# Optimization experiments

Hardware: AMD Instinct MI355X
Metric: run time of the kernel (lower is better)

Reference implementation:

```python
import jax, jax.numpy as jnp
import numpy as np
from jax import lax

H = 128  # LSTM hidden size (hardcoded in module)

def setup_inputs() -> dict:
    key = jax.random.key(0)
    ks = jax.random.split(key, 10)
    B, S, D = 256, 512, 80
    T = 3
    s_in = 1.0 / np.sqrt(D)
    s_h = 1.0 / np.sqrt(H)
    return {
        "x": jax.random.normal(ks[0], (B, S, D), dtype=jnp.float32),
        "W_in": jax.random.uniform(ks[1], (256, D), jnp.float32, -s_in, s_in),
        "b_in": jax.random.uniform(ks[2], (256,), jnp.float32, -s_in, s_in),
        "W_ih": jax.random.uniform(ks[3], (4 * H, 256), jnp.float32, -s_h, s_h),
        "b_ih": jax.random.uniform(ks[4], (4 * H,), jnp.float32, -s_h, s_h),
        "W_hh": jax.random.uniform(ks[5], (4 * H, H), jnp.float32, -s_h, s_h),
        "b_hh": jax.random.uniform(ks[6], (4 * H,), jnp.float32, -s_h, s_h),
        "w_time": jax.random.uniform(ks[7], (T,), jnp.float32, -1.0 / np.sqrt(T), 1.0 / np.sqrt(T)),
        "W_br": jax.random.uniform(ks[8], (4, H), jnp.float32, -s_h, s_h),
        "b_br": jax.random.uniform(ks[9], (4,), jnp.float32, -s_h, s_h),
        "batch_size": B,
        "time_steps": T,
    }


def reference(x, W_in, b_in, W_ih, b_ih, W_hh, b_hh, w_time, W_br, b_br, batch_size, time_steps):
    # input projection (dropout is identity in eval mode)
    xl = jnp.einsum('bsd,ed->bse', x, W_in) + b_in  # [B,S,256]
    B, S, _ = xl.shape
    T = time_steps

    def step(carry, inp):
        h, c, h_st, c_st = carry
        xt, i = inp  # xt: [B,256], i: step index
        gates = xt @ W_ih.T + b_ih + h @ W_hh.T + b_hh  # [B,4H]
        ig, fg, gg, og = jnp.split(gates, 4, axis=-1)
        c_new = jax.nn.sigmoid(fg) * c + jax.nn.sigmoid(ig) * jnp.tanh(gg)
        h_new = jax.nn.sigmoid(og) * jnp.tanh(c_new)
        slot = i % T
        oh = jax.nn.one_hot(slot, T, dtype=h_new.dtype)  # [T]
        h_st = h_st * (1.0 - oh) + h_new[:, :, None] * oh  # [B,H,T]
        c_st = c_st * (1.0 - oh) + c_new[:, :, None] * oh
        pool = (slot == T - 1)
        ph = jnp.einsum('bht,t->bh', h_st, w_time)
        pc = jnp.einsum('bht,t->bh', c_st, w_time)
        h_out = jnp.where(pool, ph, h_new)
        c_out = jnp.where(pool, pc, c_new)
        h_st = jnp.where(pool, jnp.zeros_like(h_st), h_st)
        c_st = jnp.where(pool, jnp.zeros_like(c_st), c_st)
        return (h_out, c_out, h_st, c_st), h_out

    init = (jnp.zeros((B, H), xl.dtype), jnp.zeros((B, H), xl.dtype),
            jnp.zeros((B, H, T), xl.dtype), jnp.zeros((B, H, T), xl.dtype))
    _, outs = lax.scan(step, init, (jnp.swapaxes(xl, 0, 1), jnp.arange(S)))
    out = jnp.swapaxes(outs, 0, 1)  # [B,S,H]
    logits = jnp.einsum('bsh,oh->bso', out, W_br) + b_br  # [B,S,4]
    return jax.nn.log_softmax(logits, axis=2)
```

## Files before the change

### kernel.cpp

```cpp
#include <hip/hip_runtime.h>
#include <hip/hip_fp16.h>

#define BB 256
#define SS 512
#define DD 80
#define HH 128
#define GG 512

typedef _Float16 h2_t __attribute__((ext_vector_type(2)));

union U32H2 { unsigned int u; h2_t h; unsigned short us[2]; };

static __device__ __forceinline__ h2_t u2h(unsigned int u) { U32H2 x; x.u = u; return x.h; }

static __device__ __forceinline__ unsigned int pk2(float a, float b) {
  unsigned int lo = (unsigned int)__half_as_ushort(__float2half(a));
  unsigned int hi = (unsigned int)__half_as_ushort(__float2half(b));
  return (hi << 16) | lo;
}

static __device__ __forceinline__ float fdot2(unsigned int a, unsigned int b, float c) {
#if __has_builtin(__builtin_amdgcn_fdot2)
  return __builtin_amdgcn_fdot2(u2h(a), u2h(b), c, false);
#else
  U32H2 ua, ub; ua.u = a; ub.u = b;
  return c + (float)ua.h[0] * (float)ub.h[0] + (float)ua.h[1] * (float)ub.h[1];
#endif
}

static __device__ __forceinline__ float fsig(float x) {
  return __fdividef(1.f, 1.f + __expf(-x));
}

__global__ __launch_bounds__(128) void prep_kernel(
    const float* __restrict__ W_in, const float* __restrict__ b_in,
    const float* __restrict__ W_ih, const float* __restrict__ b_ih,
    const float* __restrict__ W_hh, const float* __restrict__ b_hh,
    unsigned short* __restrict__ wc16, unsigned short* __restrict__ whh16,
    float* __restrict__ biasc)
{
  const int g = blockIdx.x;
  const int t = threadIdx.x;
  const float* wih = W_ih + g * 256;
  if (t < DD) {
    float s = 0.f;
    for (int e = 0; e < 256; ++e) s += wih[e] * W_in[e * DD + t];
    wc16[g * DD + t] = __half_as_ushort(__float2half(s));
  }
  whh16[g * HH + t] = __half_as_ushort(__float2half(W_hh[g * HH + t]));
  if (t == 0) {
    float s = 0.f;
    for (int e = 0; e < 256; ++e) s += wih[e] * b_in[e];
    biasc[g] = s + b_ih[g] + b_hh[g];
  }
}

__global__ __launch_bounds__(256) void gemm_kernel(
    const float* __restrict__ x,
    const unsigned short* __restrict__ wc16,
    uint4* __restrict__ gx)
{
  __shared__ unsigned int Al[40][64];
  __shared__ unsigned int Bl[40][256];
  const int t  = threadIdx.x;
  const int mt = blockIdx.x;
  const int g0 = blockIdx.y * 256;

  {
    const int mm = t & 63, kq = t >> 6;
    const float* xr = x + ((size_t)mt * 64 + mm) * DD + kq * 20;
    #pragma unroll
    for (int p = 0; p < 10; ++p)
      Al[kq * 10 + p][mm] = pk2(xr[2 * p], xr[2 * p + 1]);
  }
  {
    const unsigned int* wr = (const unsigned int*)wc16 + (size_t)(g0 + t) * 40;
    #pragma unroll
    for (int k = 0; k < 40; ++k) Bl[k][t] = wr[k];
  }
  __syncthreads();

  const int mb = (t >> 5) * 8;
  const int gb = (t & 31) * 4;
  float acc[8][8];
  #pragma unroll
  for (int i = 0; i < 8; ++i)
    #pragma unroll
    for (int j = 0; j < 8; ++j) acc[i][j] = 0.f;

  #pragma unroll 5
  for (int kk = 0; kk < 40; ++kk) {
    uint4 a0 = *(const uint4*)&Al[kk][mb];
    uint4 a1 = *(const uint4*)&Al[kk][mb + 4];
    uint4 b0 = *(const uint4*)&Bl[kk][gb];
    uint4 b1 = *(const uint4*)&Bl[kk][gb + 128];
    unsigned int aa[8] = {a0.x, a0.y, a0.z, a0.w, a1.x, a1.y, a1.z, a1.w};
    unsigned int bb[8] = {b0.x, b0.y, b0.z, b0.w, b1.x, b1.y, b1.z, b1.w};
    #pragma unroll
    for (int i = 0; i < 8; ++i)
      #pragma unroll
      for (int j = 0; j < 8; ++j)
        acc[i][j] = fdot2(aa[i], bb[j], acc[i][j]);
  }

  const size_t rb = (size_t)mt * 8 + (t >> 5);
  #pragma unroll
  for (int jj = 0; jj < 2; ++jj) {
    #pragma unroll
    for (int j = 0; j < 4; ++j) {
      const int jc = jj * 4 + j;
      uint4 o;
      o.x = pk2(acc[0][jc], acc[1][jc]);
      o.y = pk2(acc[2][jc], acc[3][jc]);
      o.z = pk2(acc[4][jc], acc[5][jc]);
      o.w = pk2(acc[6][jc], acc[7][jc]);
      gx[rb * 512 + (size_t)(g0 + jj * 128 + gb + j)] = o;
    }
  }
}

__global__ __launch_bounds__(256, 1) void scan_kernel(
    const uint4* __restrict__ gx,
    const uint4* __restrict__ whh,
    const float* __restrict__ biasc,
    const float* __restrict__ wtime,
    __half* __restrict__ hout)
{
  __shared__ unsigned int hbuf[2][64];
  const int b    = blockIdx.x;
  const int t    = threadIdx.x;
  const int lane = t & 63;
  const int hi   = t >> 1;
  const int odd  = t & 1;
  const int g1   = odd * 128 + hi;
  const int g2   = g1 + 256;

  unsigned int w1[64], w2[64];
  {
    const uint4* wr1 = whh + (size_t)g1 * 16;
    const uint4* wr2 = whh + (size_t)g2 * 16;
    #pragma unroll
    for (int i = 0; i < 16; ++i) {
      uint4 v = wr1[i];
      w1[4*i] = v.x; w1[4*i+1] = v.y; w1[4*i+2] = v.z; w1[4*i+3] = v.w;
      uint4 u = wr2[i];
      w2[4*i] = u.x; w2[4*i+1] = u.y; w2[4*i+2] = u.z; w2[4*i+3] = u.w;
    }
  }
  const float bias1 = biasc[g1];
  const float bias2 = biasc[g2];
  const float wt0 = wtime[0], wt1 = wtime[1], wt2 = wtime[2];
  if (t < 64) { hbuf[0][t] = 0u; hbuf[1][t] = 0u; }
  float c = 0.f, hst0 = 0.f, hst1 = 0.f, cst0 = 0.f, cst1 = 0.f;
  int slot = 0, s = 0;
  const uint4* gxp1 = gx + (size_t)b * 64 * 512 + g1;
  const uint4* gxp2 = gx + (size_t)b * 64 * 512 + g2;
  __syncthreads();

  uint4 gv1 = gxp1[0];
  uint4 gv2 = gxp2[0];
  for (int sb = 0; sb < 64; ++sb) {
    uint4 gn1, gn2;
    if (sb < 63) {
      gn1 = gxp1[(size_t)(sb + 1) * 512];
      gn2 = gxp2[(size_t)(sb + 1) * 512];
    }
    unsigned int ga1[4] = {gv1.x, gv1.y, gv1.z, gv1.w};
    unsigned int ga2[4] = {gv2.x, gv2.y, gv2.z, gv2.w};
    #pragma unroll
    for (int i = 0; i < 8; ++i) {
      const int par = s & 1;
      const unsigned int hreg = hbuf[par][lane];
      U32H2 u1; u1.u = ga1[i >> 1];
      U32H2 u2; u2.u = ga2[i >> 1];
      const float gxi1 = (float)u1.h[i & 1];
      const float gxi2 = (float)u2.h[i & 1];
      float d1a = bias1 + gxi1, d1b = 0.f;
      float d2a = bias2 + gxi2, d2b = 0.f;
      #pragma unroll
      for (int p = 0; p < 64; p += 2) {
        unsigned int h0 = (unsigned int)__builtin_amdgcn_readlane((int)hreg, p);
        unsigned int h1 = (unsigned int)__builtin_amdgcn_readlane((int)hreg, p + 1);
        d1a = fdot2(w1[p],     h0, d1a);
        d2a = fdot2(w2[p],     h0, d2a);
        d1b = fdot2(w1[p + 1], h1, d1b);
        d2b = fdot2(w2[p + 1], h1, d2b);
      }
      const float d1 = d1a + d1b;
      const float d2 = d2a + d2b;
      const float a1 = fsig(d1);
      const float yin = odd ? d2 : (d2 + d2);
      const float sv  = fsig(yin);
      const float a2  = odd ? sv : (2.f * sv - 1.f);
      const float p1 = __shfl_xor(a1, 1);
      const float p2 = __shfl_xor(a2, 1);
      const float iv = odd ? p1 : a1;
      const float gg = odd ? p2 : a2;
      const float fv = odd ? a1 : p1;
      const float ov = odd ? a2 : p2;
      c = fv * c + iv * gg;
      const float tc = 2.f * fsig(c + c) - 1.f;
      const float hn = ov * tc;
      float hcur;
      if (slot == 2) {
        hcur = hst0 * wt0 + hst1 * wt1 + hn * wt2;
        c    = cst0 * wt0 + cst1 * wt1 + c  * wt2;
        slot = 0;
      } else {
        hcur = hn;
        if (slot == 0) { hst0 = hn; cst0 = c; }
        else           { hst1 = hn; cst1 = c; }
        ++slot;
      }
      if (!odd) {
        const __half hh = __float2half(hcur);
        ((__half*)hbuf[par ^ 1])[hi] = hh;
        hout[((size_t)b * SS + s) * HH + hi] = hh;
      }
      ++s;
      __syncthreads();
    }
    gv1 = gn1;
    gv2 = gn2;
  }
}

__global__ __launch_bounds__(256) void out_kernel(
    const uint4* __restrict__ hout,
    const float* __restrict__ Wbr, const float* __restrict__ bbr,
    float4* __restrict__ out)
{
  __shared__ unsigned int wb[4][64];
  __shared__ float bbs[4];
  const int t = threadIdx.x;
  {
    const int o = t >> 6, p = t & 63;
    wb[o][p] = pk2(Wbr[o * HH + 2 * p], Wbr[o * HH + 2 * p + 1]);
  }
  if (t < 4) bbs[t] = bbr[t];
  __syncthreads();

  const size_t row = (size_t)blockIdx.x * 256 + t;
  const uint4* hr = hout + row * 16;
  float a0 = bbs[0], a1 = bbs[1], a2 = bbs[2], a3 = bbs[3];
  #pragma unroll
  for (int q = 0; q < 16; ++q) {
    uint4 hv = hr[q];
    unsigned int hd[4] = {hv.x, hv.y, hv.z, hv.w};
    #pragma unroll
    for (int d = 0; d < 4; ++d) {
      const int p = q * 4 + d;
      a0 = fdot2(hd[d], wb[0][p], a0);
      a1 = fdot2(hd[d], wb[1][p], a1);
      a2 = fdot2(hd[d], wb[2][p], a2);
      a3 = fdot2(hd[d], wb[3][p], a3);
    }
  }
  const float m = fmaxf(fmaxf(a0, a1), fmaxf(a2, a3));
  const float e0 = __expf(a0 - m), e1 = __expf(a1 - m), e2 = __expf(a2 - m), e3 = __expf(a3 - m);
  const float lse = m + __logf(e0 + e1 + e2 + e3);
  out[row] = make_float4(a0 - lse, a1 - lse, a2 - lse, a3 - lse);
}

extern "C" void kernel_launch(void* const* d_in, const int* in_sizes, int n_in,
                              void* d_out, int out_size, void* d_ws, size_t ws_size,
                              hipStream_t stream) {
  const float* x     = (const float*)d_in[0];
  const float* W_in  = (const float*)d_in[1];
  const float* b_in  = (const float*)d_in[2];
  const float* W_ih  = (const float*)d_in[3];
  const float* b_ih  = (const float*)d_in[4];
  const float* W_hh  = (const float*)d_in[5];
  const float* b_hh  = (const float*)d_in[6];
  const float* wtime = (const float*)d_in[7];
  const float* W_br  = (const float*)d_in[8];
  const float* b_br  = (const float*)d_in[9];
  (void)in_sizes; (void)n_in; (void)out_size; (void)ws_size;

  char* ws = (char*)d_ws;
  unsigned short* wc16  = (unsigned short*)(ws + 0);
  unsigned short* whh16 = (unsigned short*)(ws + 81920);
  float*          biasc = (float*)(ws + 212992);
  __half*         hout  = (__half*)(ws + 215040);
  uint4*          gx    = (uint4*)(ws + 33769472);

  prep_kernel<<<512, 128, 0, stream>>>(W_in, b_in, W_ih, b_ih, W_hh, b_hh,
                                       wc16, whh16, biasc);
  gemm_kernel<<<dim3(2048, 2), 256, 0, stream>>>(x, wc16, gx);
  scan_kernel<<<256, 256, 0, stream>>>(gx, (const uint4*)whh16, biasc, wtime, hout);
  out_kernel<<<512, 256, 0, stream>>>((const uint4*)hout, W_br, b_br, (float4*)d_out);
}
```

Baseline: 609.3 us.

## Rewrite input-gate GEMM with MFMA 16x16x32 f16 instructions

Replaces the fdot2-based register-tiled input projection GEMM with one that uses MFMA 16x16x32 f16 instructions. Shared memory is re-laid row-major with K padded from 80 to 96 using zeros, loads become vectorized float4/uint4, and each block now covers 128 gate columns across a grid twice as wide. Output packing uses a lane shuffle to keep the same interleaved gx layout. The scan kernel's occupancy hint moves from launch_bounds min-blocks to amdgpu_waves_per_eu(1,1). The GEMM is a small part of total time next to the sequential scan, so the overall effect is limited.

```diff
diff --git a/kernel.cpp b/kernel.cpp
--- a/kernel.cpp
+++ b/kernel.cpp
@@ -8,6 +8,8 @@
 #define GG 512
 
 typedef _Float16 h2_t __attribute__((ext_vector_type(2)));
+typedef _Float16 half8 __attribute__((ext_vector_type(8)));
+typedef float f32x4 __attribute__((ext_vector_type(4)));
 
 union U32H2 { unsigned int u; h2_t h; unsigned short us[2]; };
 
@@ -57,69 +59,78 @@
 
 __global__ __launch_bounds__(256) void gemm_kernel(
     const float* __restrict__ x,
-    const unsigned short* __restrict__ wc16,
+    const unsigned int* __restrict__ wc,
     uint4* __restrict__ gx)
 {
-  __shared__ unsigned int Al[40][64];
-  __shared__ unsigned int Bl[40][256];
+  __shared__ unsigned int Al[64 * 52];
+  __shared__ unsigned int Bl[128 * 52];
   const int t  = threadIdx.x;
   const int mt = blockIdx.x;
-  const int g0 = blockIdx.y * 256;
+  const int g0 = blockIdx.y * 128;
 
   {
-    const int mm = t & 63, kq = t >> 6;
-    const float* xr = x + ((size_t)mt * 64 + mm) * DD + kq * 20;
-    #pragma unroll
-    for (int p = 0; p < 10; ++p)
-      Al[kq * 10 + p][mm] = pk2(xr[2 * p], xr[2 * p + 1]);
+    const float4* xr = (const float4*)(x + (size_t)mt * 64 * DD);
+    #pragma unroll
+    for (int i = 0; i < 5; ++i) {
+      int f = t + i * 256;
+      int row = f / 20, c4 = f % 20;
+      float4 v = xr[row * 20 + c4];
+      Al[row * 52 + c4 * 2]     = pk2(v.x, v.y);
+      Al[row * 52 + c4 * 2 + 1] = pk2(v.z, v.w);
+    }
+    #pragma unroll
+    for (int i = 0; i < 3; ++i) {
+      int f = t + i * 256;
+      int row = f / 12, c = f % 12;
+      Al[row * 52 + 40 + c] = 0u;
+    }
   }
   {
-    const unsigned int* wr = (const unsigned int*)wc16 + (size_t)(g0 + t) * 40;
-    #pragma unroll
-    for (int k = 0; k < 40; ++k) Bl[k][t] = wr[k];
+    #pragma unroll
+    for (int i = 0; i < 5; ++i) {
+      int f = t + i * 256;
+      int row = f / 10, c4 = f % 10;
+      uint4 v = *(const uint4*)(wc + (size_t)(g0 + row) * 40 + c4 * 4);
+      *(uint4*)&Bl[row * 52 + c4 * 4] = v;
+    }
+    #pragma unroll
+    for (int i = 0; i < 3; ++i) {
+      int f = t + i * 256;
+      int row = f / 12, c = f % 12;
+      Bl[row * 52 + 40 + c] = 0u;
+    }
   }
   __syncthreads();
 
-  const int mb = (t >> 5) * 8;
-  const int gb = (t & 31) * 4;
-  float acc[8][8];
+  const int w = t >> 6, lane = t & 63;
+  const int m = lane & 15, q = lane >> 4;
+
+  half8 af[3];
   #pragma unroll
-  for (int i = 0; i < 8; ++i)
-    #pragma unroll
-    for (int j = 0; j < 8; ++j) acc[i][j] = 0.f;
-
-  #pragma unroll 5
-  for (int kk = 0; kk < 40; ++kk) {
-    uint4 a0 = *(const uint4*)&Al[kk][mb];
-    uint4 a1 = *(const uint4*)&Al[kk][mb + 4];
-    uint4 b0 = *(const uint4*)&Bl[kk][gb];
-    uint4 b1 = *(const uint4*)&Bl[kk][gb + 128];
-    unsigned int aa[8] = {a0.x, a0.y, a0.z, a0.w, a1.x, a1.y, a1.z, a1.w};
-    unsigned int bb[8] = {b0.x, b0.y, b0.z, b0.w, b1.x, b1.y, b1.z, b1.w};
-    #pragma unroll
-    for (int i = 0; i < 8; ++i)
-      #pragma unroll
-      for (int j = 0; j < 8; ++j)
-        acc[i][j] = fdot2(aa[i], bb[j], acc[i][j]);
-  }
-
-  const size_t rb = (size_t)mt * 8 + (t >> 5);
+  for (int kk = 0; kk < 3; ++kk)
+    af[kk] = *(const half8*)((const char*)Al + (size_t)(w * 16 + m) * 208 + kk * 64 + q * 16);
+
   #pragma unroll
-  for (int jj = 0; jj < 2; ++jj) {
-    #pragma unroll
-    for (int j = 0; j < 4; ++j) {
-      const int jc = jj * 4 + j;
-      uint4 o;
-      o.x = pk2(acc[0][jc], acc[1][jc]);
-      o.y = pk2(acc[2][jc], acc[3][jc]);
-      o.z = pk2(acc[4][jc], acc[5][jc]);
-      o.w = pk2(acc[6][jc], acc[7][jc]);
-      gx[rb * 512 + (size_t)(g0 + jj * 128 + gb + j)] = o;
-    }
-  }
-}
-
-__global__ __launch_bounds__(256, 1) void scan_kernel(
+  for (int j = 0; j < 8; ++j) {
+    f32x4 acc = {0.f, 0.f, 0.f, 0.f};
+    #pragma unroll
+    for (int kk = 0; kk < 3; ++kk) {
+      half8 bf = *(const half8*)((const char*)Bl + (size_t)(j * 16 + m) * 208 + kk * 64 + q * 16);
+      acc = __builtin_amdgcn_mfma_f32_16x16x32_f16(af[kk], bf, acc, 0, 0, 0);
+    }
+    unsigned int lo  = pk2(acc[0], acc[1]);
+    unsigned int hi  = pk2(acc[2], acc[3]);
+    unsigned int plo = (unsigned int)__shfl_down((int)lo, 16);
+    unsigned int phi = (unsigned int)__shfl_down((int)hi, 16);
+    if ((q & 1) == 0) {
+      uint4 o; o.x = lo; o.y = hi; o.z = plo; o.w = phi;
+      gx[((size_t)mt * 8 + w * 2 + (q >> 1)) * 512 + (size_t)(g0 + j * 16 + m)] = o;
+    }
+  }
+}
+
+__global__ __attribute__((amdgpu_waves_per_eu(1, 1))) __launch_bounds__(256)
+void scan_kernel(
     const uint4* __restrict__ gx,
     const uint4* __restrict__ whh,
     const float* __restrict__ biasc,
@@ -286,7 +297,7 @@
 
   prep_kernel<<<512, 128, 0, stream>>>(W_in, b_in, W_ih, b_ih, W_hh, b_hh,
                                        wc16, whh16, biasc);
-  gemm_kernel<<<dim3(2048, 2), 256, 0, stream>>>(x, wc16, gx);
+  gemm_kernel<<<dim3(2048, 4), 256, 0, stream>>>(x, (const unsigned int*)wc16, gx);
   scan_kernel<<<256, 256, 0, stream>>>(gx, (const uint4*)whh16, biasc, wtime, hout);
   out_kernel<<<512, 256, 0, stream>>>((const uint4*)hout, W_br, b_br, (float4*)d_out);
 }
```

Measured after the change: 559.9 us. 8.1% less time.
